# Kernel tuning notes

Hardware: AMD Instinct MI355X
Metric: run time of the kernel (lower is better)

## Reference

```python
import jax, jax.numpy as jnp
import numpy as np

D_MODEL = 1024
NUM_HEADS = 16
D_FF = 4096
BATCH = 4
SEQ = 1024
EPS = 1e-5
ROPE_THETA = 10000.0


def trunc_normal(key, shape):
    # approximate torch trunc_normal_(mean=0, std=1, a=-2, b=2)
    return jax.random.truncated_normal(key, -2.0, 2.0, shape, dtype=jnp.float32)


def setup_inputs() -> dict:
    key = jax.random.key(0)
    ks = jax.random.split(key, 10)
    d, h, f = D_MODEL, NUM_HEADS, D_FF
    return {
        "x": jax.random.normal(ks[0], (BATCH, SEQ, d), dtype=jnp.float32),
        "wq": trunc_normal(ks[1], (d, d)),
        "wk": trunc_normal(ks[2], (d, d)),
        "wv": trunc_normal(ks[3], (d, d)),
        "wo": trunc_normal(ks[4], (d, d)),
        "w1": trunc_normal(ks[5], (f, d)),
        "w2": trunc_normal(ks[6], (d, f)),
        "w3": trunc_normal(ks[7], (f, d)),
        "g1": trunc_normal(ks[8], (d,)),
        "g2": trunc_normal(ks[9], (d,)),
    }


def rms_norm(x, g):
    # source sums (x^2 + eps) then divides by d -> mean(x^2) + eps
    rms = jnp.sqrt(jnp.mean(jnp.square(x), axis=-1, keepdims=True) + EPS)
    return x * g / rms


def apply_rope(x, pos):
    # x: [b, h, s, d_k]; interleaved-pair rotation, theta=ROPE_THETA
    dk = x.shape[-1]
    inv_freq = ROPE_THETA ** (-jnp.arange(0, dk, 2, dtype=jnp.float32) / dk)
    ang = pos[:, None].astype(jnp.float32) * inv_freq[None, :]  # [s, dk/2]
    cos, sin = jnp.cos(ang), jnp.sin(ang)
    x1, x2 = x[..., 0::2], x[..., 1::2]
    r1 = x1 * cos - x2 * sin
    r2 = x1 * sin + x2 * cos
    return jnp.stack([r1, r2], axis=-1).reshape(x.shape)


def reference(x, wq, wk, wv, wo, w1, w2, w3, g1, g2):
    b, s, d = x.shape
    h, dk = NUM_HEADS, d // NUM_HEADS
    pos = jnp.arange(s)

    # --- attention sub-block (pre-norm) ---
    y = rms_norm(x, g1)
    q = (y @ wq.T).reshape(b, s, h, dk).transpose(0, 2, 1, 3)
    k = (y @ wk.T).reshape(b, s, h, dk).transpose(0, 2, 1, 3)
    v = (y @ wv.T).reshape(b, s, h, dk).transpose(0, 2, 1, 3)
    q = apply_rope(q, pos)
    k = apply_rope(k, pos)
    scores = jnp.einsum('bhqd,bhkd->bhqk', q, k) / jnp.sqrt(jnp.float32(dk))
    causal = jnp.tril(jnp.ones((s, s), dtype=bool))
    scores = jnp.where(causal, scores, -jnp.inf)
    attn = jax.nn.softmax(scores, axis=-1)
    ctx = jnp.einsum('bhqk,bhkd->bhqd', attn, v)
    ctx = ctx.transpose(0, 2, 1, 3).reshape(b, s, d)
    x = x + ctx @ wo.T

    # --- SwiGLU FFN sub-block (pre-norm) ---
    y = rms_norm(x, g2)
    l1 = y @ w1.T
    glu = (jax.nn.sigmoid(l1) * l1) * (y @ w3.T)
    return x + glu @ w2.T
```

## Files before the change

### kernel.cpp

```cpp
#include <hip/hip_runtime.h>

typedef __bf16 bf16;
typedef __attribute__((ext_vector_type(8))) __bf16 bf16x8;
typedef __attribute__((ext_vector_type(4))) float f32x4;

static __device__ __forceinline__ int swz4(int r) { return (r >> 1) & 3; }

static __device__ __forceinline__ void async_cp16(void* lds, const void* g) {
  __builtin_amdgcn_global_load_lds((__attribute__((address_space(1))) void*)g,
                                   (__attribute__((address_space(3))) void*)lds,
                                   16, 0, 0);
}

static __device__ __forceinline__ f32x4 mfma16(bf16x8 a, bf16x8 b, f32x4 c) {
  return __builtin_amdgcn_mfma_f32_16x16x32_bf16(a, b, c, 0, 0, 0);
}

static __device__ __forceinline__ unsigned short bfbits(float f) {
  bf16 b = (bf16)f;
  return __builtin_bit_cast(unsigned short, b);
}

extern "C" __global__ void prep_kernel(
    const float* __restrict__ wq, const float* __restrict__ wk,
    const float* __restrict__ wv, const float* __restrict__ wo,
    const float* __restrict__ w1, const float* __restrict__ w3,
    const float* __restrict__ w2,
    unsigned short* __restrict__ WQH, unsigned short* __restrict__ WQL,
    unsigned short* __restrict__ WKH, unsigned short* __restrict__ WKL,
    unsigned short* __restrict__ WVH, unsigned short* __restrict__ WOH,
    unsigned short* __restrict__ W1H, unsigned short* __restrict__ W3H,
    unsigned short* __restrict__ W2H, float2* __restrict__ rope) {
  const int seg = blockIdx.y;
  const int i = blockIdx.x * 256 + threadIdx.x;
  if (seg == 7) {
    if (i >= 32768) return;
    int s = i >> 5, fi = i & 31;
    float inv_freq = powf(10000.0f, -(2.0f * (float)fi) / 64.0f);
    float ang = (float)s * inv_freq;
    float2 cs;
    cs.x = cosf(ang);
    cs.y = sinf(ang);
    rope[i] = cs;
    return;
  }
  const float* src;
  unsigned short* hi_;
  unsigned short* lo_ = nullptr;
  int n4;
  switch (seg) {
    case 0: src = wq; hi_ = WQH; lo_ = WQL; n4 = 262144; break;
    case 1: src = wk; hi_ = WKH; lo_ = WKL; n4 = 262144; break;
    case 2: src = wv; hi_ = WVH; n4 = 262144; break;
    case 3: src = wo; hi_ = WOH; n4 = 262144; break;
    case 4: src = w1; hi_ = W1H; n4 = 1048576; break;
    case 5: src = w3; hi_ = W3H; n4 = 1048576; break;
    default: src = w2; hi_ = W2H; n4 = 1048576; break;
  }
  if (i >= n4) return;
  float4 v = ((const float4*)src)[i];
  bf16 b0 = (bf16)v.x, b1 = (bf16)v.y, b2 = (bf16)v.z, b3 = (bf16)v.w;
  ushort4 oh;
  oh.x = __builtin_bit_cast(unsigned short, b0);
  oh.y = __builtin_bit_cast(unsigned short, b1);
  oh.z = __builtin_bit_cast(unsigned short, b2);
  oh.w = __builtin_bit_cast(unsigned short, b3);
  ((ushort4*)hi_)[i] = oh;
  if (lo_) {
    ushort4 ol;
    ol.x = bfbits(v.x - (float)b0);
    ol.y = bfbits(v.y - (float)b1);
    ol.z = bfbits(v.z - (float)b2);
    ol.w = bfbits(v.w - (float)b3);
    ((ushort4*)lo_)[i] = ol;
  }
}

extern "C" __global__ __launch_bounds__(256) void rmsnorm_kernel(
    const float* __restrict__ x, const float* __restrict__ g,
    unsigned short* __restrict__ yhi, unsigned short* __restrict__ ylo) {
  int row = blockIdx.x;
  int t = threadIdx.x;
  const float4 xv = *(const float4*)(x + (size_t)row * 1024 + t * 4);
  float ss = xv.x * xv.x + xv.y * xv.y + xv.z * xv.z + xv.w * xv.w;
#pragma unroll
  for (int d = 1; d < 64; d <<= 1) ss += __shfl_xor(ss, d, 64);
  __shared__ float red[4];
  if ((t & 63) == 0) red[t >> 6] = ss;
  __syncthreads();
  float tot = red[0] + red[1] + red[2] + red[3];
  float inv = 1.0f / sqrtf(tot * (1.0f / 1024.0f) + 1e-5f);
  const float4 gv = *(const float4*)(g + t * 4);
  float y0 = xv.x * gv.x * inv, y1 = xv.y * gv.y * inv;
  float y2 = xv.z * gv.z * inv, y3 = xv.w * gv.w * inv;
  bf16 b0 = (bf16)y0, b1 = (bf16)y1, b2 = (bf16)y2, b3 = (bf16)y3;
  ushort4 oh;
  oh.x = __builtin_bit_cast(unsigned short, b0);
  oh.y = __builtin_bit_cast(unsigned short, b1);
  oh.z = __builtin_bit_cast(unsigned short, b2);
  oh.w = __builtin_bit_cast(unsigned short, b3);
  ((ushort4*)yhi)[(size_t)row * 256 + t] = oh;
  if (ylo) {
    ushort4 ol;
    ol.x = bfbits(y0 - (float)b0);
    ol.y = bfbits(y1 - (float)b1);
    ol.z = bfbits(y2 - (float)b2);
    ol.w = bfbits(y3 - (float)b3);
    ((ushort4*)ylo)[(size_t)row * 256 + t] = ol;
  }
}

template <int EPI>
__global__ __launch_bounds__(256, 2) void gemm_nt(
    const bf16* __restrict__ A, const bf16* __restrict__ B, int N, int K, int ldk,
    float* __restrict__ outF, bf16* __restrict__ outB,
    const float* __restrict__ resF) {
  const int bid = blockIdx.x;
  const int xcd = bid & 7, sq = bid >> 3;
  const int z = sq >> 5;
  const int rem = sq & 31;
  const size_t tm = (size_t)(xcd * 4 + (rem >> 3)) * 128;
  const size_t tn = (size_t)(rem & 7) * 128;
  A += (size_t)z * K;
  B += (size_t)z * K;
  __shared__ alignas(16) bf16 As[128 * 64];
  __shared__ alignas(16) bf16 Bs[128 * 64];
  const int tid = threadIdx.x;
  const int lane = tid & 63, wave = tid >> 6;
  const int lo = lane & 15, hi = lane >> 4;
  const int wm = wave >> 1, wn = wave & 1;
  f32x4 acc[4][4] = {};
  for (int k0 = 0; k0 < K; k0 += 64) {
    __syncthreads();
#pragma unroll
    for (int i4 = 0; i4 < 4; i4++) {
      int p = tid + 256 * i4;
      int row = p >> 3, c = p & 7;
      int cs = c ^ (row & 7);
      async_cp16((char*)As + (size_t)p * 16, A + (tm + row) * (size_t)ldk + k0 + cs * 8);
      async_cp16((char*)Bs + (size_t)p * 16, B + (tn + row) * (size_t)ldk + k0 + cs * 8);
    }
    __syncthreads();
#pragma unroll
    for (int kh = 0; kh < 2; kh++) {
      bf16x8 fa[4], fb[4];
#pragma unroll
      for (int i = 0; i < 4; i++) {
        int ra = wm * 64 + i * 16 + lo;
        fa[i] = *(const bf16x8*)((const char*)As + ra * 128 + (((kh * 4 + hi) ^ (ra & 7)) << 4));
        int rb = wn * 64 + i * 16 + lo;
        fb[i] = *(const bf16x8*)((const char*)Bs + rb * 128 + (((kh * 4 + hi) ^ (rb & 7)) << 4));
      }
      __builtin_amdgcn_s_setprio(1);
#pragma unroll
      for (int i = 0; i < 4; i++)
#pragma unroll
        for (int j = 0; j < 4; j++) acc[i][j] = mfma16(fa[i], fb[j], acc[i][j]);
      __builtin_amdgcn_s_setprio(0);
    }
  }
#pragma unroll
  for (int i = 0; i < 4; i++)
#pragma unroll
    for (int j = 0; j < 4; j++)
#pragma unroll
      for (int r = 0; r < 4; r++) {
        size_t m = tm + wm * 64 + i * 16 + hi * 4 + r;
        size_t n = tn + wn * 64 + j * 16 + lo;
        float v = acc[i][j][r];
        if constexpr (EPI == 0) {
          size_t idx = (((m >> 10) * 16 + (n >> 6)) * 64 + (n & 63)) * 1024 + (m & 1023);
          outB[idx] = (bf16)v;
        } else if constexpr (EPI == 1) {
          size_t idx = m * (size_t)N + n;
          outF[idx] = v + resF[idx];
        } else {
          atomicAdd(&outF[m * (size_t)N + n], v);
        }
      }
}

extern "C" __global__ __launch_bounds__(512, 2) void gemm_up_kernel(
    const bf16* __restrict__ A, const bf16* __restrict__ B1,
    const bf16* __restrict__ B3, bf16* __restrict__ G) {
  __shared__ alignas(16) bf16 LA[2][2][256][32];
  __shared__ alignas(16) bf16 LB1[2][2][128][32];
  __shared__ alignas(16) bf16 LB3[2][2][128][32];
  const int tid = threadIdx.x;
  const int lane = tid & 63, wave = tid >> 6;
  const int lo = lane & 15, hi = lane >> 4;
  const int wm = wave >> 1, wn = wave & 1;
  const int bid = blockIdx.x;
  const int xcd = bid & 7, sq = bid >> 3;
  const size_t tn = (size_t)(xcd * 4 + (sq & 3)) * 128;
  const size_t tm = (size_t)(sq >> 2) * 256;

  f32x4 acc1[4][4] = {}, acc3[4][4] = {};

  int offA[4], offB[4];
#pragma unroll
  for (int i = 0; i < 4; i++) {
    int ra = wm * 64 + i * 16 + lo;
    offA[i] = ra * 64 + ((hi ^ swz4(ra)) << 4);
    int rb = wn * 64 + i * 16 + lo;
    offB[i] = rb * 64 + ((hi ^ swz4(rb)) << 4);
  }

  const int r0 = tid >> 2, c0 = tid & 3;
  const bf16* pA0 = A + (tm + r0) * (size_t)1024 + ((c0 ^ swz4(r0)) << 3);
  const bf16* pB1 = B1 + (tn + r0) * (size_t)1024 + ((c0 ^ swz4(r0)) << 3);
  const bf16* pB3 = B3 + (tn + r0) * (size_t)1024 + ((c0 ^ swz4(r0)) << 3);

  auto stA = [&](char* plane) {
    async_cp16(plane + tid * 16, pA0);
    async_cp16(plane + (512 + tid) * 16, pA0 + 128 * 1024);
    pA0 += 32;
  };
  auto stB = [&](char* plane1, char* plane3) {
    async_cp16(plane1 + tid * 16, pB1);
    pB1 += 32;
    async_cp16(plane3 + tid * 16, pB3);
    pB3 += 32;
  };

  stA((char*)&LA[0][0][0][0]); stB((char*)&LB1[0][0][0][0], (char*)&LB3[0][0][0][0]);
  stA((char*)&LA[0][1][0][0]); stB((char*)&LB1[0][1][0][0], (char*)&LB3[0][1][0][0]);
  stA((char*)&LA[1][0][0][0]); stB((char*)&LB1[1][0][0][0], (char*)&LB3[1][0][0][0]);
  asm volatile("s_waitcnt vmcnt(4)");
  __builtin_amdgcn_s_barrier();

#define UP_RD(ARR, P, KH, OFF) \
  (*(const bf16x8*)((const char*)&ARR[P][KH][0][0] + (OFF)))

#define UP_MFMA(ACC)                                        \
  __builtin_amdgcn_s_setprio(1);                            \
  _Pragma("unroll") for (int i = 0; i < 4; i++)             \
    _Pragma("unroll") for (int j = 0; j < 4; j++)           \
      ACC[i][j] = mfma16(fa[i], fb[j], ACC[i][j]);          \
  __builtin_amdgcn_s_setprio(0);

#define UP_TILE(T, P)                                                          \
  {                                                                            \
    bf16x8 fa[4], fb[4];                                                       \
    _Pragma("unroll") for (int i = 0; i < 4; i++) {                            \
      fa[i] = UP_RD(LA, P, 0, offA[i]);                                        \
      fb[i] = UP_RD(LB1, P, 0, offB[i]);                                       \
    }                                                                          \
    if ((T) + 1 < 16) stA((char*)&LA[(P) ^ 1][1][0][0]);                       \
    UP_MFMA(acc1)                                                              \
    __builtin_amdgcn_s_barrier();                                              \
    _Pragma("unroll") for (int j = 0; j < 4; j++)                              \
      fb[j] = UP_RD(LB3, P, 0, offB[j]);                                       \
    if ((T) + 1 < 16)                                                          \
      stB((char*)&LB1[(P) ^ 1][1][0][0], (char*)&LB3[(P) ^ 1][1][0][0]);       \
    UP_MFMA(acc3)                                                              \
    __builtin_amdgcn_s_barrier();                                              \
    _Pragma("unroll") for (int i = 0; i < 4; i++) {                            \
      fa[i] = UP_RD(LA, P, 1, offA[i]);                                        \
      fb[i] = UP_RD(LB1, P, 1, offB[i]);                                       \
    }                                                                          \
    if ((T) + 2 < 16) stA((char*)&LA[P][0][0][0]);                             \
    UP_MFMA(acc1)                                                              \
    __builtin_amdgcn_s_barrier();                                              \
    _Pragma("unroll") for (int j = 0; j < 4; j++)                              \
      fb[j] = UP_RD(LB3, P, 1, offB[j]);                                       \
    if ((T) + 2 < 16)                                                          \
      stB((char*)&LB1[P][0][0][0], (char*)&LB3[P][0][0][0]);                   \
    UP_MFMA(acc3)                                                              \
    if ((T) + 2 < 16) {                                                        \
      asm volatile("s_waitcnt vmcnt(4)");                                      \
    } else if ((T) + 1 < 16) {                                                 \
      asm volatile("s_waitcnt vmcnt(0)");                                      \
    }                                                                          \
    __builtin_amdgcn_s_barrier();                                              \
  }

  for (int tt = 0; tt < 16; tt += 2) {
    UP_TILE(tt, 0)
    UP_TILE(tt + 1, 1)
  }

#pragma unroll
  for (int i = 0; i < 4; i++)
#pragma unroll
    for (int j = 0; j < 4; j++)
#pragma unroll
      for (int r = 0; r < 4; r++) {
        size_t m = tm + wm * 64 + i * 16 + hi * 4 + r;
        size_t n = tn + wn * 64 + j * 16 + lo;
        float v1 = acc1[i][j][r], v3 = acc3[i][j][r];
        G[m * 4096 + n] = (bf16)(v1 / (1.0f + __expf(-v1)) * v3);
      }
}

extern "C" __global__ __launch_bounds__(256, 2) void gemm_qk_kernel(
    const bf16* __restrict__ Ah, const bf16* __restrict__ Al,
    const bf16* __restrict__ BhQ, const bf16* __restrict__ BlQ,
    const bf16* __restrict__ BhK, const bf16* __restrict__ BlK,
    const float2* __restrict__ rope,
    bf16* __restrict__ OhQ, bf16* __restrict__ OlQ,
    bf16* __restrict__ OhK, bf16* __restrict__ OlK) {
  const int bid = blockIdx.x;
  const int xcd = bid & 7, sq = bid >> 3;
  const int zqk = sq >> 5;
  const int rem = sq & 31;
  const size_t tm = (size_t)(xcd * 4 + (rem >> 3)) * 128;
  const size_t tn = (size_t)(rem & 7) * 128;
  const bf16* Bh = zqk ? BhK : BhQ;
  const bf16* Bl = zqk ? BlK : BlQ;
  bf16* Oh = zqk ? OhK : OhQ;
  bf16* Ol = zqk ? OlK : OlQ;
  __shared__ alignas(16) bf16 Ahs[128 * 64], Als[128 * 64];
  __shared__ alignas(16) bf16 Bhs[128 * 64], Bls[128 * 64];
  const int tid = threadIdx.x;
  const int lane = tid & 63, wave = tid >> 6;
  const int lo = lane & 15, hi = lane >> 4;
  const int wm = wave >> 1, wn = wave & 1;
  const int K = 1024;
  f32x4 acc[4][4] = {};
  for (int k0 = 0; k0 < K; k0 += 64) {
    __syncthreads();
#pragma unroll
    for (int i4 = 0; i4 < 4; i4++) {
      int p = tid + 256 * i4;
      int row = p >> 3, c = p & 7;
      int cs = c ^ (row & 7);
      size_t ga = (tm + row) * (size_t)K + k0 + cs * 8;
      size_t gb = (tn + row) * (size_t)K + k0 + cs * 8;
      async_cp16((char*)Ahs + (size_t)p * 16, Ah + ga);
      async_cp16((char*)Als + (size_t)p * 16, Al + ga);
      async_cp16((char*)Bhs + (size_t)p * 16, Bh + gb);
      async_cp16((char*)Bls + (size_t)p * 16, Bl + gb);
    }
    __syncthreads();
#pragma unroll
    for (int kh = 0; kh < 2; kh++) {
      int offa[4], offb[4];
#pragma unroll
      for (int i = 0; i < 4; i++) {
        int ra = wm * 64 + i * 16 + lo;
        offa[i] = ra * 128 + (((kh * 4 + hi) ^ (ra & 7)) << 4);
        int rb = wn * 64 + i * 16 + lo;
        offb[i] = rb * 128 + (((kh * 4 + hi) ^ (rb & 7)) << 4);
      }
      bf16x8 fah[4], fbh[4], fx[4];
#pragma unroll
      for (int i = 0; i < 4; i++) {
        fah[i] = *(const bf16x8*)((const char*)Ahs + offa[i]);
        fbh[i] = *(const bf16x8*)((const char*)Bhs + offb[i]);
      }
      __builtin_amdgcn_s_setprio(1);
#pragma unroll
      for (int i = 0; i < 4; i++)
#pragma unroll
        for (int j = 0; j < 4; j++) acc[i][j] = mfma16(fah[i], fbh[j], acc[i][j]);
      __builtin_amdgcn_s_setprio(0);
#pragma unroll
      for (int j = 0; j < 4; j++) fx[j] = *(const bf16x8*)((const char*)Bls + offb[j]);
      __builtin_amdgcn_s_setprio(1);
#pragma unroll
      for (int i = 0; i < 4; i++)
#pragma unroll
        for (int j = 0; j < 4; j++) acc[i][j] = mfma16(fah[i], fx[j], acc[i][j]);
      __builtin_amdgcn_s_setprio(0);
#pragma unroll
      for (int i = 0; i < 4; i++) fx[i] = *(const bf16x8*)((const char*)Als + offa[i]);
      __builtin_amdgcn_s_setprio(1);
#pragma unroll
      for (int i = 0; i < 4; i++)
#pragma unroll
        for (int j = 0; j < 4; j++) acc[i][j] = mfma16(fx[i], fbh[j], acc[i][j]);
      __builtin_amdgcn_s_setprio(0);
    }
  }
#pragma unroll
  for (int i = 0; i < 4; i++)
#pragma unroll
    for (int j = 0; j < 4; j++)
#pragma unroll
      for (int r = 0; r < 4; r++) {
        float v = acc[i][j][r];
        float vp = __shfl_xor(v, 1, 64);
        size_t m = tm + wm * 64 + i * 16 + hi * 4 + r;
        size_t n = tn + wn * 64 + j * 16 + lo;
        int s = (int)(m & 1023);
        int pi = (int)((n & 63) >> 1);
        float2 cs = rope[s * 32 + pi];
        float res = (n & 1) ? (vp * cs.y + v * cs.x) : (v * cs.x - vp * cs.y);
        size_t idx = (((m >> 10) * 16 + (n >> 6)) * 1024 + (m & 1023)) * 64 + (n & 63);
        bf16 hb = (bf16)res;
        Oh[idx] = hb;
        Ol[idx] = (bf16)(res - (float)hb);
      }
}

extern "C" __global__ __launch_bounds__(256, 4) void flash_kernel(
    const bf16* __restrict__ qhi, const bf16* __restrict__ qlo,
    const bf16* __restrict__ khi, const bf16* __restrict__ klo,
    const bf16* __restrict__ vT, bf16* __restrict__ ctx) {
  const int bid = blockIdx.x;
  const int qb = bid >> 6;
  const int bh = bid & 63;
  const int tid = threadIdx.x;
  const int wave = tid >> 6, lane = tid & 63;
  const int lo = lane & 15, hi = lane >> 4;

  __shared__ alignas(16) bf16 Ksh[2][64][32];
  __shared__ alignas(16) bf16 Ksl[2][64][32];
  __shared__ alignas(16) bf16 Vs[2][64][32];
  __shared__ alignas(16) bf16 P[4][16][72];

  size_t qoff = ((size_t)bh * 1024 + qb * 64 + wave * 16 + lo) * 64;
  bf16x8 qh[2], ql[2];
#pragma unroll
  for (int ks = 0; ks < 2; ks++) {
    qh[ks] = *(const bf16x8*)(qhi + qoff + ks * 32 + hi * 8);
    ql[ks] = *(const bf16x8*)(qlo + qoff + ks * 32 + hi * 8);
  }

  const int srow = tid >> 2;
  const int scl = (tid & 3) ^ swz4(srow);
  const size_t kgb = (size_t)bh * 1024 * 64;
  const size_t vgb = ((size_t)bh * 64 + srow) * 1024;

  float mrun[4] = {-1e30f, -1e30f, -1e30f, -1e30f};
  float lrun[4] = {0.f, 0.f, 0.f, 0.f};
  f32x4 o[4] = {};
  const float scale = 0.125f;

  for (int kt = 0; kt <= qb; kt++) {
    __syncthreads();
#pragma unroll
    for (int i = 0; i < 2; i++) {
      int p = tid + 256 * i;
      size_t gk = kgb + (size_t)(kt * 64 + srow) * 64 + i * 32 + scl * 8;
      async_cp16((char*)Ksh + (size_t)p * 16, khi + gk);
      async_cp16((char*)Ksl + (size_t)p * 16, klo + gk);
      async_cp16((char*)Vs + (size_t)p * 16, vT + vgb + kt * 64 + i * 32 + scl * 8);
    }
    __syncthreads();

    f32x4 sv[4];
    __builtin_amdgcn_s_setprio(1);
#pragma unroll
    for (int nb = 0; nb < 4; nb++) {
      f32x4 a = {0.f, 0.f, 0.f, 0.f};
#pragma unroll
      for (int ks = 0; ks < 2; ks++) {
        int row = nb * 16 + lo;
        int off16 = (ks * 64 + row) * 4 + (hi ^ swz4(row));
        bf16x8 kh = *(const bf16x8*)((const char*)Ksh + off16 * 16);
        bf16x8 kl = *(const bf16x8*)((const char*)Ksl + off16 * 16);
        a = mfma16(qh[ks], kh, a);
        a = mfma16(qh[ks], kl, a);
        a = mfma16(ql[ks], kh, a);
      }
      sv[nb] = a;
    }
    __builtin_amdgcn_s_setprio(0);

    const bool mt = (kt == qb);
#pragma unroll
    for (int nb = 0; nb < 4; nb++)
#pragma unroll
      for (int r = 0; r < 4; r++) {
        float s = sv[nb][r] * scale;
        if (mt) {
          int kp = nb * 16 + lo;
          int qr = wave * 16 + hi * 4 + r;
          if (kp > qr) s = -1e30f;
        }
        sv[nb][r] = s;
      }
    float mnew[4], rs[4];
#pragma unroll
    for (int r = 0; r < 4; r++) {
      float mx = fmaxf(fmaxf(sv[0][r], sv[1][r]), fmaxf(sv[2][r], sv[3][r]));
#pragma unroll
      for (int d = 1; d < 16; d <<= 1) mx = fmaxf(mx, __shfl_xor(mx, d, 64));
      mnew[r] = fmaxf(mrun[r], mx);
      float sc = __expf(mrun[r] - mnew[r]);
      lrun[r] *= sc;
#pragma unroll
      for (int db = 0; db < 4; db++) o[db][r] *= sc;
      mrun[r] = mnew[r];
      rs[r] = 0.f;
    }
#pragma unroll
    for (int nb = 0; nb < 4; nb++)
#pragma unroll
      for (int r = 0; r < 4; r++) {
        float p = __expf(sv[nb][r] - mnew[r]);
        bf16 pb = (bf16)p;
        rs[r] += (float)pb;
        P[wave][hi * 4 + r][nb * 16 + lo] = pb;
      }
#pragma unroll
    for (int r = 0; r < 4; r++) {
      float t = rs[r];
#pragma unroll
      for (int d = 1; d < 16; d <<= 1) t += __shfl_xor(t, d, 64);
      lrun[r] += t;
    }
    bf16x8 pa[2];
#pragma unroll
    for (int ks = 0; ks < 2; ks++) pa[ks] = *(const bf16x8*)&P[wave][lo][ks * 32 + hi * 8];
    __builtin_amdgcn_s_setprio(1);
#pragma unroll
    for (int db = 0; db < 4; db++)
#pragma unroll
      for (int ks = 0; ks < 2; ks++) {
        int row = db * 16 + lo;
        int off16 = (ks * 64 + row) * 4 + (hi ^ swz4(row));
        bf16x8 vf = *(const bf16x8*)((const char*)Vs + off16 * 16);
        o[db] = mfma16(pa[ks], vf, o[db]);
      }
    __builtin_amdgcn_s_setprio(0);
  }
  int b = bh >> 4, h = bh & 15;
#pragma unroll
  for (int db = 0; db < 4; db++)
#pragma unroll
    for (int r = 0; r < 4; r++) {
      float val = o[db][r] / lrun[r];
      size_t row = (size_t)b * 1024 + qb * 64 + wave * 16 + hi * 4 + r;
      ctx[row * 1024 + h * 64 + db * 16 + lo] = (bf16)val;
    }
}


extern "C" void kernel_launch(void* const* d_in, const int* in_sizes, int n_in,
                              void* d_out, int out_size, void* d_ws, size_t ws_size,
                              hipStream_t stream) {
  (void)in_sizes; (void)n_in; (void)out_size; (void)ws_size;
  const float* x  = (const float*)d_in[0];
  const float* wq = (const float*)d_in[1];
  const float* wk = (const float*)d_in[2];
  const float* wv = (const float*)d_in[3];
  const float* wo = (const float*)d_in[4];
  const float* w1 = (const float*)d_in[5];
  const float* w2 = (const float*)d_in[6];
  const float* w3 = (const float*)d_in[7];
  const float* g1 = (const float*)d_in[8];
  const float* g2 = (const float*)d_in[9];
  float* out = (float*)d_out;

  char* ws = (char*)d_ws;
  size_t off = 0;
  auto alloc = [&](size_t bytes) {
    char* p = ws + off;
    off += (bytes + 255) & ~(size_t)255;
    return p;
  };
  const size_t MB2 = 1024u * 1024u * 2u;
  const size_t MB8 = 4096u * 1024u * 2u;
  void* WQH = alloc(MB2);  void* WQL = alloc(MB2);
  void* WKH = alloc(MB2);  void* WKL = alloc(MB2);
  void* WVH = alloc(MB2);  void* WOH = alloc(MB2);
  void* W1H = alloc(MB8);  void* W3H = alloc(MB8);  void* W2H = alloc(MB8);
  void* ROPE = alloc(32768u * 8u);
  void* Y1H = alloc(MB8);  void* Y1L = alloc(MB8);
  void* QH = alloc(MB8);   void* QL = alloc(MB8);
  void* KH = alloc(MB8);   void* KL = alloc(MB8);
  void* VT = alloc(MB8);
  void* CTX = alloc(MB8);
  void* Y2H = alloc(MB8);
  void* GLU = QH;

  prep_kernel<<<dim3(4096, 8), dim3(256), 0, stream>>>(
      wq, wk, wv, wo, w1, w3, w2,
      (unsigned short*)WQH, (unsigned short*)WQL, (unsigned short*)WKH,
      (unsigned short*)WKL, (unsigned short*)WVH, (unsigned short*)WOH,
      (unsigned short*)W1H, (unsigned short*)W3H, (unsigned short*)W2H,
      (float2*)ROPE);

  rmsnorm_kernel<<<dim3(4096), dim3(256), 0, stream>>>(
      x, g1, (unsigned short*)Y1H, (unsigned short*)Y1L);

  gemm_qk_kernel<<<dim3(512), dim3(256), 0, stream>>>(
      (const bf16*)Y1H, (const bf16*)Y1L,
      (const bf16*)WQH, (const bf16*)WQL, (const bf16*)WKH, (const bf16*)WKL,
      (const float2*)ROPE,
      (bf16*)QH, (bf16*)QL, (bf16*)KH, (bf16*)KL);

  gemm_nt<0><<<dim3(256), dim3(256), 0, stream>>>(
      (const bf16*)Y1H, (const bf16*)WVH, 1024, 1024, 1024,
      nullptr, (bf16*)VT, nullptr);

  flash_kernel<<<dim3(1024), dim3(256), 0, stream>>>(
      (const bf16*)QH, (const bf16*)QL, (const bf16*)KH, (const bf16*)KL,
      (const bf16*)VT, (bf16*)CTX);

  gemm_nt<1><<<dim3(256), dim3(256), 0, stream>>>(
      (const bf16*)CTX, (const bf16*)WOH, 1024, 1024, 1024,
      out, nullptr, x);

  rmsnorm_kernel<<<dim3(4096), dim3(256), 0, stream>>>(
      out, g2, (unsigned short*)Y2H, nullptr);

  gemm_up_kernel<<<dim3(512), dim3(512), 0, stream>>>(
      (const bf16*)Y2H, (const bf16*)W1H, (const bf16*)W3H, (bf16*)GLU);

  gemm_nt<5><<<dim3(1024), dim3(256), 0, stream>>>(
      (const bf16*)GLU, (const bf16*)W2H, 1024, 1024, 4096,
      out, nullptr, nullptr);
}
```

Before: 310.1 us.

## Replace pipelined 256x128 SwiGLU up-GEMM with simple 128x128 single-buffered loop

Rewrites the fused W1/W3 up-projection kernel to use 128x128 tiles with 256 threads and a 64-wide K step, loading all operands into a single swizzled LDS buffer each iteration. The hand-scheduled double-buffered pipeline with interleaved async loads and partial waits is removed. The launch grid doubles to cover the smaller tiles. This trades load/compute overlap and larger-tile operand reuse for simpler code and more blocks.

After: 305.4 us. No clear change (-1.5%).

```diff
diff --git a/kernel.cpp b/kernel.cpp
--- a/kernel.cpp
+++ b/kernel.cpp
@@ -180,106 +180,62 @@
       }
 }
 
-extern "C" __global__ __launch_bounds__(512, 2) void gemm_up_kernel(
+extern "C" __global__ __launch_bounds__(256, 2) void gemm_up_kernel(
     const bf16* __restrict__ A, const bf16* __restrict__ B1,
     const bf16* __restrict__ B3, bf16* __restrict__ G) {
-  __shared__ alignas(16) bf16 LA[2][2][256][32];
-  __shared__ alignas(16) bf16 LB1[2][2][128][32];
-  __shared__ alignas(16) bf16 LB3[2][2][128][32];
+  const int bid = blockIdx.x;
+  const int xcd = bid & 7, sq = bid >> 3;
+  const size_t tm = (size_t)(xcd * 4 + (sq & 3)) * 128;
+  const size_t tn = (size_t)(sq >> 2) * 128;
+  __shared__ alignas(16) bf16 As[128 * 64];
+  __shared__ alignas(16) bf16 B1s[128 * 64];
+  __shared__ alignas(16) bf16 B3s[128 * 64];
   const int tid = threadIdx.x;
   const int lane = tid & 63, wave = tid >> 6;
   const int lo = lane & 15, hi = lane >> 4;
   const int wm = wave >> 1, wn = wave & 1;
-  const int bid = blockIdx.x;
-  const int xcd = bid & 7, sq = bid >> 3;
-  const size_t tn = (size_t)(xcd * 4 + (sq & 3)) * 128;
-  const size_t tm = (size_t)(sq >> 2) * 256;
-
   f32x4 acc1[4][4] = {}, acc3[4][4] = {};
-
-  int offA[4], offB[4];
-#pragma unroll
-  for (int i = 0; i < 4; i++) {
-    int ra = wm * 64 + i * 16 + lo;
-    offA[i] = ra * 64 + ((hi ^ swz4(ra)) << 4);
-    int rb = wn * 64 + i * 16 + lo;
-    offB[i] = rb * 64 + ((hi ^ swz4(rb)) << 4);
-  }
-
-  const int r0 = tid >> 2, c0 = tid & 3;
-  const bf16* pA0 = A + (tm + r0) * (size_t)1024 + ((c0 ^ swz4(r0)) << 3);
-  const bf16* pB1 = B1 + (tn + r0) * (size_t)1024 + ((c0 ^ swz4(r0)) << 3);
-  const bf16* pB3 = B3 + (tn + r0) * (size_t)1024 + ((c0 ^ swz4(r0)) << 3);
-
-  auto stA = [&](char* plane) {
-    async_cp16(plane + tid * 16, pA0);
-    async_cp16(plane + (512 + tid) * 16, pA0 + 128 * 1024);
-    pA0 += 32;
-  };
-  auto stB = [&](char* plane1, char* plane3) {
-    async_cp16(plane1 + tid * 16, pB1);
-    pB1 += 32;
-    async_cp16(plane3 + tid * 16, pB3);
-    pB3 += 32;
-  };
-
-  stA((char*)&LA[0][0][0][0]); stB((char*)&LB1[0][0][0][0], (char*)&LB3[0][0][0][0]);
-  stA((char*)&LA[0][1][0][0]); stB((char*)&LB1[0][1][0][0], (char*)&LB3[0][1][0][0]);
-  stA((char*)&LA[1][0][0][0]); stB((char*)&LB1[1][0][0][0], (char*)&LB3[1][0][0][0]);
-  asm volatile("s_waitcnt vmcnt(4)");
-  __builtin_amdgcn_s_barrier();
-
-#define UP_RD(ARR, P, KH, OFF) \
-  (*(const bf16x8*)((const char*)&ARR[P][KH][0][0] + (OFF)))
-
-#define UP_MFMA(ACC)                                        \
-  __builtin_amdgcn_s_setprio(1);                            \
-  _Pragma("unroll") for (int i = 0; i < 4; i++)             \
-    _Pragma("unroll") for (int j = 0; j < 4; j++)           \
-      ACC[i][j] = mfma16(fa[i], fb[j], ACC[i][j]);          \
-  __builtin_amdgcn_s_setprio(0);
-
-#define UP_TILE(T, P)                                                          \
-  {                                                                            \
-    bf16x8 fa[4], fb[4];                                                       \
-    _Pragma("unroll") for (int i = 0; i < 4; i++) {                            \
-      fa[i] = UP_RD(LA, P, 0, offA[i]);                                        \
-      fb[i] = UP_RD(LB1, P, 0, offB[i]);                                       \
-    }                                                                          \
-    if ((T) + 1 < 16) stA((char*)&LA[(P) ^ 1][1][0][0]);                       \
-    UP_MFMA(acc1)                                                              \
-    __builtin_amdgcn_s_barrier();                                              \
-    _Pragma("unroll") for (int j = 0; j < 4; j++)                              \
-      fb[j] = UP_RD(LB3, P, 0, offB[j]);                                       \
-    if ((T) + 1 < 16)                                                          \
-      stB((char*)&LB1[(P) ^ 1][1][0][0], (char*)&LB3[(P) ^ 1][1][0][0]);       \
-    UP_MFMA(acc3)                                                              \
-    __builtin_amdgcn_s_barrier();                                              \
-    _Pragma("unroll") for (int i = 0; i < 4; i++) {                            \
-      fa[i] = UP_RD(LA, P, 1, offA[i]);                                        \
-      fb[i] = UP_RD(LB1, P, 1, offB[i]);                                       \
-    }                                                                          \
-    if ((T) + 2 < 16) stA((char*)&LA[P][0][0][0]);                             \
-    UP_MFMA(acc1)                                                              \
-    __builtin_amdgcn_s_barrier();                                              \
-    _Pragma("unroll") for (int j = 0; j < 4; j++)                              \
-      fb[j] = UP_RD(LB3, P, 1, offB[j]);                                       \
-    if ((T) + 2 < 16)                                                          \
-      stB((char*)&LB1[P][0][0][0], (char*)&LB3[P][0][0][0]);                   \
-    UP_MFMA(acc3)                                                              \
-    if ((T) + 2 < 16) {                                                        \
-      asm volatile("s_waitcnt vmcnt(4)");                                      \
-    } else if ((T) + 1 < 16) {                                                 \
-      asm volatile("s_waitcnt vmcnt(0)");                                      \
-    }                                                                          \
-    __builtin_amdgcn_s_barrier();                                              \
-  }
-
-  for (int tt = 0; tt < 16; tt += 2) {
-    UP_TILE(tt, 0)
-    UP_TILE(tt + 1, 1)
-  }
-
+  for (int k0 = 0; k0 < 1024; k0 += 64) {
+    __syncthreads();
+#pragma unroll
+    for (int i4 = 0; i4 < 4; i4++) {
+      int p = tid + 256 * i4;
+      int row = p >> 3, c = p & 7;
+      int cs = c ^ (row & 7);
+      async_cp16((char*)As + (size_t)p * 16, A + (tm + row) * (size_t)1024 + k0 + cs * 8);
+      async_cp16((char*)B1s + (size_t)p * 16, B1 + (tn + row) * (size_t)1024 + k0 + cs * 8);
+      async_cp16((char*)B3s + (size_t)p * 16, B3 + (tn + row) * (size_t)1024 + k0 + cs * 8);
+    }
+    __syncthreads();
+#pragma unroll
+    for (int kh = 0; kh < 2; kh++) {
+      bf16x8 fa[4], fb[4];
+#pragma unroll
+      for (int i = 0; i < 4; i++) {
+        int ra = wm * 64 + i * 16 + lo;
+        fa[i] = *(const bf16x8*)((const char*)As + ra * 128 + (((kh * 4 + hi) ^ (ra & 7)) << 4));
+        int rb = wn * 64 + i * 16 + lo;
+        fb[i] = *(const bf16x8*)((const char*)B1s + rb * 128 + (((kh * 4 + hi) ^ (rb & 7)) << 4));
+      }
+      __builtin_amdgcn_s_setprio(1);
+#pragma unroll
+      for (int i = 0; i < 4; i++)
+#pragma unroll
+        for (int j = 0; j < 4; j++) acc1[i][j] = mfma16(fa[i], fb[j], acc1[i][j]);
+      __builtin_amdgcn_s_setprio(0);
+#pragma unroll
+      for (int j = 0; j < 4; j++) {
+        int rb = wn * 64 + j * 16 + lo;
+        fb[j] = *(const bf16x8*)((const char*)B3s + rb * 128 + (((kh * 4 + hi) ^ (rb & 7)) << 4));
+      }
+      __builtin_amdgcn_s_setprio(1);
+#pragma unroll
+      for (int i = 0; i < 4; i++)
+#pragma unroll
+        for (int j = 0; j < 4; j++) acc3[i][j] = mfma16(fa[i], fb[j], acc3[i][j]);
+      __builtin_amdgcn_s_setprio(0);
+    }
+  }
 #pragma unroll
   for (int i = 0; i < 4; i++)
 #pragma unroll
@@ -598,7 +554,7 @@
   rmsnorm_kernel<<<dim3(4096), dim3(256), 0, stream>>>(
       out, g2, (unsigned short*)Y2H, nullptr);
 
-  gemm_up_kernel<<<dim3(512), dim3(512), 0, stream>>>(
+  gemm_up_kernel<<<dim3(1024), dim3(256), 0, stream>>>(
       (const bf16*)Y2H, (const bf16*)W1H, (const bf16*)W3H, (bf16*)GLU);
 
   gemm_nt<5><<<dim3(1024), dim3(256), 0, stream>>>(
```
